# Kernel tuning notes

Hardware: AMD Instinct MI355X
Metric: run time of the kernel (lower is better)

## Reference

```python
import jax, jax.numpy as jnp
import numpy as np

N_DRUG = 50000
N_PROT = 50000
N_EDGE = 800000
D_IN = 256
D_HID = 256
D_OUT = 128


def setup_inputs() -> dict:
    key = jax.random.key(0)
    ks = jax.random.split(key, 20)
    s_in = 1.0 / np.sqrt(D_IN)
    inp = {
        'x_drug': jax.random.normal(ks[0], (N_DRUG, D_IN), jnp.float32),
        'x_protein': jax.random.normal(ks[1], (N_PROT, D_IN), jnp.float32),
        'edge_dp': jnp.stack([
            jax.random.randint(ks[2], (N_EDGE,), 0, N_DRUG, jnp.int32),
            jax.random.randint(ks[3], (N_EDGE,), 0, N_PROT, jnp.int32)]),
        'edge_pd': jnp.stack([
            jax.random.randint(ks[4], (N_EDGE,), 0, N_PROT, jnp.int32),
            jax.random.randint(ks[5], (N_EDGE,), 0, N_DRUG, jnp.int32)]),
        'W1l_dp': jax.random.normal(ks[6], (D_IN, D_HID), jnp.float32) * s_in,
        'W1r_dp': jax.random.normal(ks[7], (D_IN, D_HID), jnp.float32) * s_in,
        'b1_dp': jnp.zeros((D_HID,), jnp.float32),
        'W1l_pd': jax.random.normal(ks[8], (D_IN, D_HID), jnp.float32) * s_in,
        'W1r_pd': jax.random.normal(ks[9], (D_IN, D_HID), jnp.float32) * s_in,
        'b1_pd': jnp.zeros((D_HID,), jnp.float32),
        'W2l_dp': jax.random.normal(ks[10], (D_HID, D_OUT), jnp.float32) / np.sqrt(D_HID),
        'W2r_dp': jax.random.normal(ks[11], (D_HID, D_OUT), jnp.float32) / np.sqrt(D_HID),
        'b2_dp': jnp.zeros((D_OUT,), jnp.float32),
        'W2l_pd': jax.random.normal(ks[12], (D_HID, D_OUT), jnp.float32) / np.sqrt(D_HID),
        'W2r_pd': jax.random.normal(ks[13], (D_HID, D_OUT), jnp.float32) / np.sqrt(D_HID),
        'b2_pd': jnp.zeros((D_OUT,), jnp.float32),
    }
    return inp


def _sage(x_src, x_dst, edge, Wl, Wr, b):
    """PyG SAGEConv (mean aggr): lin_l(mean_neighbors) + lin_r(x_dst) + bias."""
    src, dst = edge[0], edge[1]
    n_dst = x_dst.shape[0]
    msg = x_src[src]                                        # [E, d] gather
    s = jax.ops.segment_sum(msg, dst, num_segments=n_dst)   # [n_dst, d]
    cnt = jax.ops.segment_sum(jnp.ones((edge.shape[1],), x_src.dtype), dst,
                              num_segments=n_dst)
    mean = s / jnp.maximum(cnt, 1.0)[:, None]
    return mean @ Wl + x_dst @ Wr + b


def _l2norm(x, eps=1e-12):
    n = jnp.sqrt(jnp.sum(x * x, axis=-1, keepdims=True))
    return x / jnp.maximum(n, eps)


def reference(x_drug, x_protein, edge_dp, edge_pd,
              W1l_dp, W1r_dp, b1_dp, W1l_pd, W1r_pd, b1_pd,
              W2l_dp, W2r_dp, b2_dp, W2l_pd, W2r_pd, b2_pd):
    # Layer 1 (HeteroConv, aggr='sum'; each node type has one incoming edge type)
    h_prot = _sage(x_drug, x_protein, edge_dp, W1l_dp, W1r_dp, b1_dp)
    h_drug = _sage(x_protein, x_drug, edge_pd, W1l_pd, W1r_pd, b1_pd)
    h_prot = jax.nn.relu(h_prot)  # dropout is identity in eval mode
    h_drug = jax.nn.relu(h_drug)
    # Layer 2 (output layer) + L2 normalize
    z_prot = _sage(h_drug, h_prot, edge_dp, W2l_dp, W2r_dp, b2_dp)
    z_drug = _sage(h_prot, h_drug, edge_pd, W2l_pd, W2r_pd, b2_pd)
    return _l2norm(z_drug), _l2norm(z_prot)
```

## Files before the change

kernel.cpp:

```cpp
#include <hip/hip_runtime.h>

typedef unsigned short u16;
typedef unsigned int u32;
typedef __attribute__((ext_vector_type(8))) short short8;
typedef __attribute__((ext_vector_type(4))) float f32x4;

#define NDIM 256
#define KCAT 512
#define EB 8192
#define NBK_MAX 256

__device__ __forceinline__ float bf2f(u16 u) {
  union { u32 i; float f; } v; v.i = ((u32)u) << 16; return v.f;
}
__device__ __forceinline__ u16 f2bf(float f) {
  union { float f; u32 i; } v; v.f = f;
  u32 u = v.i;
  u32 r = (u + 0x7fffu + ((u >> 16) & 1u)) >> 16;
  return (u16)r;
}

__global__ void cvt_f32_bf16_2(const float* __restrict__ a, int n4a,
                               const float* __restrict__ b, int n4b,
                               u16* __restrict__ oa, u16* __restrict__ ob) {
  int i = blockIdx.x * blockDim.x + threadIdx.x;
  const float* in; u16* out; int j;
  if (i < n4a) { in = a; out = oa; j = i; }
  else { j = i - n4a; if (j >= n4b) return; in = b; out = ob; }
  const float4 v = reinterpret_cast<const float4*>(in)[j];
  u32 lo = (u32)f2bf(v.x) | ((u32)f2bf(v.y) << 16);
  u32 hi = (u32)f2bf(v.z) | ((u32)f2bf(v.w) << 16);
  reinterpret_cast<uint2*>(out)[j] = make_uint2(lo, hi);
}

__global__ void prep_wcat(const float* __restrict__ Wl0, const float* __restrict__ Wr0,
                          u16* __restrict__ WT0,
                          const float* __restrict__ Wl1, const float* __restrict__ Wr1,
                          u16* __restrict__ WT1) {
  int idx = blockIdx.x * blockDim.x + threadIdx.x;
  if (idx >= 256 * KCAT) return;
  const float* Wl = blockIdx.y ? Wl1 : Wl0;
  const float* Wr = blockIdx.y ? Wr1 : Wr0;
  u16* WT = blockIdx.y ? WT1 : WT0;
  int n = idx >> 9, k = idx & 511;
  float v = (k < 256) ? Wl[k * 256 + n] : Wr[(k - 256) * 256 + n];
  WT[idx] = f2bf(v);
}

__global__ void prep_wcat2(const float* __restrict__ Wl0, const float* __restrict__ Wr0,
                           u16* __restrict__ WT0,
                           const float* __restrict__ Wl1, const float* __restrict__ Wr1,
                           u16* __restrict__ WT1) {
  int idx = blockIdx.x * blockDim.x + threadIdx.x;
  if (idx >= 256 * 256) return;
  const float* Wl = blockIdx.y ? Wl1 : Wl0;
  const float* Wr = blockIdx.y ? Wr1 : Wr0;
  u16* WT = blockIdx.y ? WT1 : WT0;
  int n = idx >> 8, k = idx & 255;
  float v = (n < 128) ? Wl[k * 128 + n] : Wr[k * 128 + (n - 128)];
  WT[idx] = f2bf(v);
}

__global__ void prep_fbias(const float* __restrict__ bd, const float* __restrict__ bp,
                           float* __restrict__ fd, float* __restrict__ fp) {
  int n = threadIdx.x;
  fd[n] = (n < 128) ? 0.f : bd[n - 128];
  fp[n] = (n < 128) ? 0.f : bp[n - 128];
}

#define SCAN_CHUNK 2048

__global__ void scan_p1(const int* __restrict__ c0, int n0,
                        const int* __restrict__ c1, int n1,
                        int* __restrict__ bsums) {
  const int sel = blockIdx.y;
  const int* c = sel ? c1 : c0;
  const int n = sel ? n1 : n0;
  const int base = blockIdx.x * SCAN_CHUNK;
  const int tid = threadIdx.x, lane = tid & 63, w = tid >> 6;
  int s = 0;
  const int i0 = base + tid * 8;
#pragma unroll
  for (int j = 0; j < 8; ++j) {
    int i = i0 + j;
    s += (i < n) ? c[i] : 0;
  }
#pragma unroll
  for (int d = 1; d < 64; d <<= 1) s += __shfl_xor(s, d, 64);
  __shared__ int wsum[4];
  if (lane == 0) wsum[w] = s;
  __syncthreads();
  if (tid == 0) bsums[sel * 64 + blockIdx.x] = wsum[0] + wsum[1] + wsum[2] + wsum[3];
}

__global__ void scan_p2(int* __restrict__ bsums, int nb) {
  const int sel = blockIdx.x;
  const int lane = threadIdx.x;
  int v = (lane < nb) ? bsums[sel * 64 + lane] : 0;
#pragma unroll
  for (int d = 1; d < 64; d <<= 1) {
    int t = __shfl_up(v, d, 64);
    if (lane >= d) v += t;
  }
  int ex = __shfl_up(v, 1, 64);
  if (lane == 0) ex = 0;
  if (lane < nb) bsums[sel * 64 + lane] = ex;
}

__global__ void scan_p3(const int* __restrict__ c0, int n0, int* __restrict__ off0,
                        const int* __restrict__ c1, int n1, int* __restrict__ off1,
                        const int* __restrict__ bsums) {
  const int sel = blockIdx.y;
  const int* c = sel ? c1 : c0;
  int* off = sel ? off1 : off0;
  const int n = sel ? n1 : n0;
  const int base = blockIdx.x * SCAN_CHUNK;
  const int tid = threadIdx.x, lane = tid & 63, w = tid >> 6;
  int v[8];
  int s = 0;
  const int i0 = base + tid * 8;
#pragma unroll
  for (int j = 0; j < 8; ++j) {
    int i = i0 + j;
    v[j] = (i < n) ? c[i] : 0;
    s += v[j];
  }
  int inc = s;
#pragma unroll
  for (int d = 1; d < 64; d <<= 1) {
    int t = __shfl_up(inc, d, 64);
    if (lane >= d) inc += t;
  }
  __shared__ int wsum[4];
  if (lane == 63) wsum[w] = inc;
  __syncthreads();
  int wbase = 0;
  for (int q = 0; q < w; ++q) wbase += wsum[q];
  int run = (inc - s) + wbase + bsums[sel * 64 + blockIdx.x];
#pragma unroll
  for (int j = 0; j < 8; ++j) {
    int i = i0 + j;
    run += v[j];
    if (i < n) off[i + 1] = run;
  }
  if (blockIdx.x == 0 && tid == 0) off[0] = 0;
}

__global__ void hist_pass(const int* __restrict__ d0, const int* __restrict__ d1, int E,
                          int nblk, int nbuckets, int* __restrict__ h0, int* __restrict__ h1) {
  const int sel = blockIdx.y;
  const int* dst = sel ? d1 : d0;
  int* hist = sel ? h1 : h0;
  const int blk = blockIdx.x;
  __shared__ int h[NBK_MAX];
  for (int b = threadIdx.x; b < nbuckets; b += 256) h[b] = 0;
  __syncthreads();
  const int e0 = blk * EB;
  const int e1 = (e0 + EB < E) ? (e0 + EB) : E;
  for (int i = e0 + threadIdx.x; i < e1; i += 256) atomicAdd(&h[dst[i] >> 8], 1);
  __syncthreads();
  for (int b = threadIdx.x; b < nbuckets; b += 256) hist[b * nblk + blk] = h[b];
}

__global__ void part_pass(const int* __restrict__ s0, const int* __restrict__ d0, u32* __restrict__ t0,
                          const int* __restrict__ s1, const int* __restrict__ d1, u32* __restrict__ t1,
                          const int* __restrict__ ho0, const int* __restrict__ ho1,
                          int E, int nblk, int nbuckets) {
  const int sel = blockIdx.y;
  const int* src = sel ? s1 : s0;
  const int* dst = sel ? d1 : d0;
  const int* hoff = sel ? ho1 : ho0;
  u32* tmp = sel ? t1 : t0;
  const int blk = blockIdx.x;
  __shared__ int cur[NBK_MAX];
  for (int b = threadIdx.x; b < nbuckets; b += 256) cur[b] = hoff[b * nblk + blk];
  __syncthreads();
  const int e0 = blk * EB;
  const int e1 = (e0 + EB < E) ? (e0 + EB) : E;
  for (int i = e0 + threadIdx.x; i < e1; i += 256) {
    const int d = dst[i];
    const int p = atomicAdd(&cur[d >> 8], 1);
    tmp[p] = ((u32)(d & 255) << 16) | (u32)src[i];
  }
}

__global__ void bucket_fill(const u32* __restrict__ t0, const int* __restrict__ ho0,
                            int n0, int* __restrict__ off0, int* __restrict__ l0,
                            const u32* __restrict__ t1, const int* __restrict__ ho1,
                            int n1, int* __restrict__ off1, int* __restrict__ l1,
                            int E, int nblk, int nbuckets) {
  const int sel = blockIdx.y;
  const u32* tmp = sel ? t1 : t0;
  const int* hoff = sel ? ho1 : ho0;
  const int n = sel ? n1 : n0;
  int* off = sel ? off1 : off0;
  int* lst = sel ? l1 : l0;
  const int b = blockIdx.x;
  const int node0 = b << 8;
  if (node0 >= n) return;
  const int nodes = (n - node0 < 256) ? (n - node0) : 256;
  const int base = hoff[b * nblk];
  const int bend = hoff[(b + 1) * nblk];
  const int t = threadIdx.x, lane = t & 63, w = t >> 6;
  __shared__ int cnt[256];
  __shared__ int wsum[4];
  cnt[t] = 0;
  __syncthreads();
  for (int i = base + t; i < bend; i += 256) atomicAdd(&cnt[tmp[i] >> 16], 1);
  __syncthreads();
  const int v = cnt[t];
  int inc = v;
#pragma unroll
  for (int d = 1; d < 64; d <<= 1) {
    int x = __shfl_up(inc, d, 64);
    if (lane >= d) inc += x;
  }
  if (lane == 63) wsum[w] = inc;
  __syncthreads();
  int wb = 0;
  for (int q = 0; q < w; ++q) wb += wsum[q];
  const int excl = base + (inc - v) + wb;
  __syncthreads();
  cnt[t] = excl;
  if (t < nodes) off[node0 + t] = excl;
  if (node0 + nodes == n && t == 0) off[n] = E;
  __syncthreads();
  for (int i = base + t; i < bend; i += 256) {
    const u32 pk = tmp[i];
    const int p = atomicAdd(&cnt[pk >> 16], 1);
    lst[p] = (int)(pk & 0xffffu);
  }
}

__global__ void seg_mean(const u16* __restrict__ f0, const int* __restrict__ o0,
                         const int* __restrict__ l0, u16* __restrict__ out0, int n0,
                         const u16* __restrict__ f1, const int* __restrict__ o1,
                         const int* __restrict__ l1, u16* __restrict__ out1, int n1) {
  const int sel = blockIdx.y;
  const u16* feat = sel ? f1 : f0;
  const int* off = sel ? o1 : o0;
  const int* lst = sel ? l1 : l0;
  u16* out = sel ? out1 : out0;
  const int ndst = sel ? n1 : n0;
  const int wid = threadIdx.x >> 6, lane = threadIdx.x & 63;
  const int node = blockIdx.x * 4 + wid;
  if (node >= ndst) return;
  const int s = off[node], e = off[node + 1];
  const int half = lane >> 5, hl = lane & 31;
  float a[8];
#pragma unroll
  for (int j = 0; j < 8; ++j) a[j] = 0.f;
  int i = s;
  for (; i + 16 <= e; i += 16) {
    int q[8];
#pragma unroll
    for (int j = 0; j < 8; ++j) q[j] = lst[i + 2 * j + half];
    uint4 v[8];
#pragma unroll
    for (int j = 0; j < 8; ++j)
      v[j] = *reinterpret_cast<const uint4*>(feat + (size_t)q[j] * NDIM + hl * 8);
#pragma unroll
    for (int j = 0; j < 8; ++j) {
      const u32 w[4] = {v[j].x, v[j].y, v[j].z, v[j].w};
#pragma unroll
      for (int c = 0; c < 4; ++c) {
        a[2 * c] += bf2f((u16)(w[c] & 0xffffu));
        a[2 * c + 1] += bf2f((u16)(w[c] >> 16));
      }
    }
  }
  for (; i + 8 <= e; i += 8) {
    int q[4];
#pragma unroll
    for (int j = 0; j < 4; ++j) q[j] = lst[i + 2 * j + half];
    uint4 v[4];
#pragma unroll
    for (int j = 0; j < 4; ++j)
      v[j] = *reinterpret_cast<const uint4*>(feat + (size_t)q[j] * NDIM + hl * 8);
#pragma unroll
    for (int j = 0; j < 4; ++j) {
      const u32 w[4] = {v[j].x, v[j].y, v[j].z, v[j].w};
#pragma unroll
      for (int c = 0; c < 4; ++c) {
        a[2 * c] += bf2f((u16)(w[c] & 0xffffu));
        a[2 * c + 1] += bf2f((u16)(w[c] >> 16));
      }
    }
  }
  for (; i < e; i += 2) {
    if (i + half < e) {
      const int q = lst[i + half];
      const uint4 v = *reinterpret_cast<const uint4*>(feat + (size_t)q * NDIM + hl * 8);
      const u32 w[4] = {v.x, v.y, v.z, v.w};
#pragma unroll
      for (int c = 0; c < 4; ++c) {
        a[2 * c] += bf2f((u16)(w[c] & 0xffffu));
        a[2 * c + 1] += bf2f((u16)(w[c] >> 16));
      }
    }
  }
#pragma unroll
  for (int j = 0; j < 8; ++j) a[j] += __shfl_xor(a[j], 32, 64);
  if (half == 0) {
    const float inv = (e > s) ? 1.f / (float)(e - s) : 0.f;
    uint4 o;
    o.x = (u32)f2bf(a[0] * inv) | ((u32)f2bf(a[1] * inv) << 16);
    o.y = (u32)f2bf(a[2] * inv) | ((u32)f2bf(a[3] * inv) << 16);
    o.z = (u32)f2bf(a[4] * inv) | ((u32)f2bf(a[5] * inv) << 16);
    o.w = (u32)f2bf(a[6] * inv) | ((u32)f2bf(a[7] * inv) << 16);
    *reinterpret_cast<uint4*>(out + (size_t)node * NDIM + hl * 8) = o;
  }
}

__global__ void seg_out(const u16* __restrict__ ym0, const u16* __restrict__ ys0,
                        const int* __restrict__ o0, const int* __restrict__ l0,
                        float* __restrict__ z0, int n0,
                        const u16* __restrict__ ym1, const u16* __restrict__ ys1,
                        const int* __restrict__ o1, const int* __restrict__ l1,
                        float* __restrict__ z1, int n1) {
  const int sel = blockIdx.y;
  const u16* ymsg = sel ? ym1 : ym0;
  const u16* yself = sel ? ys1 : ys0;
  const int* off = sel ? o1 : o0;
  const int* lst = sel ? l1 : l0;
  float* zout = sel ? z1 : z0;
  const int ndst = sel ? n1 : n0;
  const int wid = threadIdx.x >> 6, lane = threadIdx.x & 63;
  const int node = blockIdx.x * 4 + wid;
  if (node >= ndst) return;
  const int s = off[node], e = off[node + 1];
  const int q = lane >> 4, ql = lane & 15;
  float a[8];
#pragma unroll
  for (int j = 0; j < 8; ++j) a[j] = 0.f;
  int i = s;
  for (; i + 16 <= e; i += 16) {
    int r[4];
#pragma unroll
    for (int j = 0; j < 4; ++j) r[j] = lst[i + 4 * j + q];
    uint4 v[4];
#pragma unroll
    for (int j = 0; j < 4; ++j)
      v[j] = *reinterpret_cast<const uint4*>(ymsg + (size_t)r[j] * 256 + ql * 8);
#pragma unroll
    for (int j = 0; j < 4; ++j) {
      const u32 w[4] = {v[j].x, v[j].y, v[j].z, v[j].w};
#pragma unroll
      for (int c = 0; c < 4; ++c) {
        a[2 * c] += bf2f((u16)(w[c] & 0xffffu));
        a[2 * c + 1] += bf2f((u16)(w[c] >> 16));
      }
    }
  }
  for (; i + 4 <= e; i += 4) {
    const int r = lst[i + q];
    const uint4 v = *reinterpret_cast<const uint4*>(ymsg + (size_t)r * 256 + ql * 8);
    const u32 w[4] = {v.x, v.y, v.z, v.w};
#pragma unroll
    for (int c = 0; c < 4; ++c) {
      a[2 * c] += bf2f((u16)(w[c] & 0xffffu));
      a[2 * c + 1] += bf2f((u16)(w[c] >> 16));
    }
  }
  if (i + q < e) {
    const int r = lst[i + q];
    const uint4 v = *reinterpret_cast<const uint4*>(ymsg + (size_t)r * 256 + ql * 8);
    const u32 w[4] = {v.x, v.y, v.z, v.w};
#pragma unroll
    for (int c = 0; c < 4; ++c) {
      a[2 * c] += bf2f((u16)(w[c] & 0xffffu));
      a[2 * c + 1] += bf2f((u16)(w[c] >> 16));
    }
  }
#pragma unroll
  for (int j = 0; j < 8; ++j) {
    a[j] += __shfl_xor(a[j], 16, 64);
    a[j] += __shfl_xor(a[j], 32, 64);
  }
  const float inv = (e > s) ? 1.f / (float)(e - s) : 0.f;
  const uint4 r = *reinterpret_cast<const uint4*>(yself + (size_t)node * 256 + 128 + ql * 8);
  const u32 rw[4] = {r.x, r.y, r.z, r.w};
  float z[8];
  float ss = 0.f;
#pragma unroll
  for (int c = 0; c < 4; ++c) {
    z[2 * c] = a[2 * c] * inv + bf2f((u16)(rw[c] & 0xffffu));
    z[2 * c + 1] = a[2 * c + 1] * inv + bf2f((u16)(rw[c] >> 16));
    ss += z[2 * c] * z[2 * c] + z[2 * c + 1] * z[2 * c + 1];
  }
#pragma unroll
  for (int d = 1; d < 16; d <<= 1) ss += __shfl_xor(ss, d, 64);
  const float sc = 1.f / fmaxf(sqrtf(ss), 1e-12f);
  if (q == 0) {
    float4 o0v, o1v;
    o0v.x = z[0] * sc; o0v.y = z[1] * sc; o0v.z = z[2] * sc; o0v.w = z[3] * sc;
    o1v.x = z[4] * sc; o1v.y = z[5] * sc; o1v.z = z[6] * sc; o1v.w = z[7] * sc;
    float* zp = zout + (size_t)node * 128 + ql * 8;
    *reinterpret_cast<float4*>(zp) = o0v;
    *reinterpret_cast<float4*>(zp + 4) = o1v;
  }
}

template <bool RELU, bool CAT, int KT, typename OutT>
__global__ __launch_bounds__(256) void gemm_cat2(
    const u16* __restrict__ Am0, const u16* __restrict__ Ax0,
    const u16* __restrict__ WT0, const float* __restrict__ bias0,
    OutT* __restrict__ out0, int M0,
    const u16* __restrict__ Am1, const u16* __restrict__ Ax1,
    const u16* __restrict__ WT1, const float* __restrict__ bias1,
    OutT* __restrict__ out1, int M1,
    int ldb, int ldo) {
  const int sel = blockIdx.z;
  const u16* Am = sel ? Am1 : Am0;
  const u16* Ax = sel ? Ax1 : Ax0;
  const u16* WT = sel ? WT1 : WT0;
  const float* bias = sel ? bias1 : bias0;
  OutT* out = sel ? out1 : out0;
  const int M = sel ? M1 : M0;
  const int gm0 = blockIdx.x * 128;
  if (gm0 >= M) return;

  __shared__ u16 As[8 * 128 * 8];
  __shared__ u16 Bs[8 * 128 * 8];
  const int tid = threadIdx.x;
  const int wid = tid >> 6, lane = tid & 63;
  const int wr = wid >> 1, wc = wid & 1;
  const int n0 = blockIdx.y * 128;

  f32x4 acc[4][4];
  const f32x4 zz = {0.f, 0.f, 0.f, 0.f};
#pragma unroll
  for (int i = 0; i < 4; ++i)
#pragma unroll
    for (int j = 0; j < 4; ++j) acc[i][j] = zz;

  for (int kt = 0; kt < KT; ++kt) {
    const u16* Asrc = CAT ? ((kt < KT / 2) ? Am : Ax) : Am;
    const int koff = CAT ? ((kt & (KT / 2 - 1)) * 64) : kt * 64;
#pragma unroll
    for (int t = 0; t < 4; ++t) {
      int f = wid * 256 + t * 64 + lane;
      int c = f >> 7, r = f & 127;
      int grow = gm0 + r; grow = (grow < M) ? grow : (M - 1);
      const u16* g = Asrc + (size_t)grow * NDIM + koff + c * 8;
      u16* l = &As[(size_t)(wid * 256 + t * 64) * 8];
      __builtin_amdgcn_global_load_lds((const __attribute__((address_space(1))) void*)g,
                                       (__attribute__((address_space(3))) void*)l, 16, 0, 0);
    }
#pragma unroll
    for (int t = 0; t < 4; ++t) {
      int f = wid * 256 + t * 64 + lane;
      int c = f >> 7, n = f & 127;
      const u16* g = WT + (size_t)(n0 + n) * ldb + kt * 64 + c * 8;
      u16* l = &Bs[(size_t)(wid * 256 + t * 64) * 8];
      __builtin_amdgcn_global_load_lds((const __attribute__((address_space(1))) void*)g,
                                       (__attribute__((address_space(3))) void*)l, 16, 0, 0);
    }
    __syncthreads();
#pragma unroll
    for (int ks = 0; ks < 2; ++ks) {
      const int kc = ks * 4 + (lane >> 4);
      short8 a[4], b[4];
#pragma unroll
      for (int mt = 0; mt < 4; ++mt)
        a[mt] = *reinterpret_cast<const short8*>(
            &As[(size_t)(kc * 128 + wr * 64 + mt * 16 + (lane & 15)) * 8]);
#pragma unroll
      for (int nt = 0; nt < 4; ++nt)
        b[nt] = *reinterpret_cast<const short8*>(
            &Bs[(size_t)(kc * 128 + wc * 64 + nt * 16 + (lane & 15)) * 8]);
#pragma unroll
      for (int mt = 0; mt < 4; ++mt)
#pragma unroll
        for (int nt = 0; nt < 4; ++nt)
          acc[mt][nt] = __builtin_amdgcn_mfma_f32_16x16x32_bf16(a[mt], b[nt], acc[mt][nt], 0, 0, 0);
    }
    __syncthreads();
  }

  const int rw = gm0 + wr * 64;
#pragma unroll
  for (int mt = 0; mt < 4; ++mt) {
#pragma unroll
    for (int j = 0; j < 4; ++j) {
      int row = rw + mt * 16 + ((lane >> 4) << 2) + j;
      if (row >= M) continue;
#pragma unroll
      for (int nt = 0; nt < 4; ++nt) {
        int col = n0 + wc * 64 + nt * 16 + (lane & 15);
        float v = acc[mt][nt][j] + bias[col];
        if (RELU) v = fmaxf(v, 0.f);
        if constexpr (sizeof(OutT) == 2) out[(size_t)row * ldo + col] = f2bf(v);
        else out[(size_t)row * ldo + col] = v;
      }
    }
  }
}

extern "C" void kernel_launch(void* const* d_in, const int* in_sizes, int n_in,
                              void* d_out, int out_size, void* d_ws, size_t ws_size,
                              hipStream_t stream) {
  const float* x_drug = (const float*)d_in[0];
  const float* x_prot = (const float*)d_in[1];
  const int* e_dp = (const int*)d_in[2];
  const int* e_pd = (const int*)d_in[3];
  const float* W1l_dp = (const float*)d_in[4];
  const float* W1r_dp = (const float*)d_in[5];
  const float* b1_dp = (const float*)d_in[6];
  const float* W1l_pd = (const float*)d_in[7];
  const float* W1r_pd = (const float*)d_in[8];
  const float* b1_pd = (const float*)d_in[9];
  const float* W2l_dp = (const float*)d_in[10];
  const float* W2r_dp = (const float*)d_in[11];
  const float* b2_dp = (const float*)d_in[12];
  const float* W2l_pd = (const float*)d_in[13];
  const float* W2r_pd = (const float*)d_in[14];
  const float* b2_pd = (const float*)d_in[15];

  const int E = in_sizes[2] / 2;
  const int ND = in_sizes[0] / NDIM;
  const int NP = in_sizes[1] / NDIM;

  const int* dp_src = e_dp;
  const int* dp_dst = e_dp + E;
  const int* pd_src = e_pd;
  const int* pd_dst = e_pd + E;

  char* ws = (char*)d_ws;
  size_t o = 0;
  auto alloc = [&](size_t bytes) -> void* {
    void* p = ws + o;
    o = (o + bytes + 255) & ~(size_t)255;
    return p;
  };
  u16* xd16 = (u16*)alloc((size_t)ND * NDIM * 2);
  u16* xp16 = (u16*)alloc((size_t)NP * NDIM * 2);
  u16* mp16 = (u16*)alloc((size_t)NP * NDIM * 2);
  u16* md16 = (u16*)alloc((size_t)ND * NDIM * 2);
  u16* hp16 = (u16*)alloc((size_t)NP * NDIM * 2);
  u16* hd16 = (u16*)alloc((size_t)ND * NDIM * 2);
  u16* wt1dp = (u16*)alloc((size_t)256 * KCAT * 2);
  u16* wt1pd = (u16*)alloc((size_t)256 * KCAT * 2);
  u16* wt2d = (u16*)alloc((size_t)256 * 256 * 2);
  u16* wt2p = (u16*)alloc((size_t)256 * 256 * 2);
  float* fbias_d = (float*)alloc(256 * 4);
  float* fbias_p = (float*)alloc(256 * 4);
  int* off_dp = (int*)alloc((size_t)(NP + 1) * 4);
  int* off_pd = (int*)alloc((size_t)(ND + 1) * 4);
  int* bsums2 = (int*)alloc((size_t)2 * 64 * 4);
  int* lst_dp = (int*)alloc((size_t)E * 4);
  int* lst_pd = (int*)alloc((size_t)E * 4);
  u32* tmp_dp = (u32*)alloc((size_t)E * 4);
  u32* tmp_pd = (u32*)alloc((size_t)E * 4);

  const int nmax = (NP > ND) ? NP : ND;
  const int nbuckets = (nmax + 255) >> 8;
  const int nblk = (E + EB - 1) / EB;
  const int nh = nbuckets * nblk;
  int* hist0 = (int*)alloc((size_t)nh * 4);
  int* hist1 = (int*)alloc((size_t)nh * 4);
  int* hoff0 = (int*)alloc((size_t)(nh + 1) * 4);
  int* hoff1 = (int*)alloc((size_t)(nh + 1) * 4);

  dim3 blk(256);

  const int n4d = ND * NDIM / 4, n4p = NP * NDIM / 4;
  cvt_f32_bf16_2<<<(n4d + n4p + 255) / 256, blk, 0, stream>>>(x_drug, n4d, x_prot, n4p, xd16, xp16);

  prep_wcat<<<dim3((256 * KCAT + 255) / 256, 2), blk, 0, stream>>>(
      W1l_dp, W1r_dp, wt1dp, W1l_pd, W1r_pd, wt1pd);
  prep_wcat2<<<dim3((256 * 256 + 255) / 256, 2), blk, 0, stream>>>(
      W2l_dp, W2r_pd, wt2d, W2l_pd, W2r_dp, wt2p);
  prep_fbias<<<1, 256, 0, stream>>>(b2_pd, b2_dp, fbias_d, fbias_p);

  hist_pass<<<dim3(nblk, 2), blk, 0, stream>>>(dp_dst, pd_dst, E, nblk, nbuckets, hist0, hist1);
  const int nb2 = (nh + SCAN_CHUNK - 1) / SCAN_CHUNK;
  dim3 sg2(nb2, 2);
  scan_p1<<<sg2, blk, 0, stream>>>(hist0, nh, hist1, nh, bsums2);
  scan_p2<<<2, 64, 0, stream>>>(bsums2, nb2);
  scan_p3<<<sg2, blk, 0, stream>>>(hist0, nh, hoff0, hist1, nh, hoff1, bsums2);
  part_pass<<<dim3(nblk, 2), blk, 0, stream>>>(
      dp_src, dp_dst, tmp_dp, pd_src, pd_dst, tmp_pd, hoff0, hoff1, E, nblk, nbuckets);
  bucket_fill<<<dim3(nbuckets, 2), blk, 0, stream>>>(
      tmp_dp, hoff0, NP, off_dp, lst_dp, tmp_pd, hoff1, ND, off_pd, lst_pd, E, nblk, nbuckets);

  seg_mean<<<dim3((nmax + 3) / 4, 2), blk, 0, stream>>>(
      xd16, off_dp, lst_dp, mp16, NP, xp16, off_pd, lst_pd, md16, ND);

  const int gx = (nmax + 127) / 128;
  gemm_cat2<true, true, 8, u16><<<dim3(gx, 2, 2), blk, 0, stream>>>(
      mp16, xp16, wt1dp, b1_dp, hp16, NP,
      md16, xd16, wt1pd, b1_pd, hd16, ND, KCAT, 256);

  u16* yp16 = mp16;
  u16* yd16 = md16;
  gemm_cat2<false, false, 4, u16><<<dim3(gx, 2, 2), blk, 0, stream>>>(
      hd16, hd16, wt2d, fbias_d, yd16, ND,
      hp16, hp16, wt2p, fbias_p, yp16, NP, 256, 256);

  float* zd = (float*)d_out;
  float* zp = zd + (size_t)ND * 128;
  seg_out<<<dim3((nmax + 3) / 4, 2), blk, 0, stream>>>(
      yp16, yd16, off_pd, lst_pd, zd, ND, yd16, yp16, off_dp, lst_dp, zp, NP);
}
```

Before: 406.1 us.

## Split feature matrices into two 128-column halves for cache-friendly gathers

Input features and intermediate buffers are stored as separate low and high 128-column halves. The neighbor-mean gather now runs as two passes, each touching a half-size table, so each pass's working set fits the cache better. The layer-2 GEMM writes its message and self outputs into separate compact buffers, and seg_out reads 128-wide rows. The cost is an extra kernel launch, an index-list reread in the second gather pass, and more pointer plumbing in the GEMM.

New measurement: 421.6 us. +3.8%, slower.

```diff
diff --git a/kernel.cpp b/kernel.cpp
--- a/kernel.cpp
+++ b/kernel.cpp
@@ -20,17 +20,20 @@
   return (u16)r;
 }
 
-__global__ void cvt_f32_bf16_2(const float* __restrict__ a, int n4a,
-                               const float* __restrict__ b, int n4b,
-                               u16* __restrict__ oa, u16* __restrict__ ob) {
+__global__ void cvt_split_2(const float* __restrict__ a, int n4a,
+                            const float* __restrict__ b, int n4b,
+                            u16* __restrict__ alo, u16* __restrict__ ahi,
+                            u16* __restrict__ blo, u16* __restrict__ bhi) {
   int i = blockIdx.x * blockDim.x + threadIdx.x;
-  const float* in; u16* out; int j;
-  if (i < n4a) { in = a; out = oa; j = i; }
-  else { j = i - n4a; if (j >= n4b) return; in = b; out = ob; }
+  const float* in; u16* lo; u16* hi; int j;
+  if (i < n4a) { in = a; lo = alo; hi = ahi; j = i; }
+  else { j = i - n4a; if (j >= n4b) return; in = b; lo = blo; hi = bhi; }
   const float4 v = reinterpret_cast<const float4*>(in)[j];
-  u32 lo = (u32)f2bf(v.x) | ((u32)f2bf(v.y) << 16);
-  u32 hi = (u32)f2bf(v.z) | ((u32)f2bf(v.w) << 16);
-  reinterpret_cast<uint2*>(out)[j] = make_uint2(lo, hi);
+  u32 w0 = (u32)f2bf(v.x) | ((u32)f2bf(v.y) << 16);
+  u32 w1 = (u32)f2bf(v.z) | ((u32)f2bf(v.w) << 16);
+  const int node = j >> 6, c4 = (j & 63) * 4;
+  u16* out = (c4 < 128) ? (lo + (size_t)node * 128 + c4) : (hi + (size_t)node * 128 + c4 - 128);
+  *reinterpret_cast<uint2*>(out) = make_uint2(w0, w1);
 }
 
 __global__ void prep_wcat(const float* __restrict__ Wl0, const float* __restrict__ Wr0,
@@ -232,10 +235,10 @@
   }
 }
 
-__global__ void seg_mean(const u16* __restrict__ f0, const int* __restrict__ o0,
-                         const int* __restrict__ l0, u16* __restrict__ out0, int n0,
-                         const u16* __restrict__ f1, const int* __restrict__ o1,
-                         const int* __restrict__ l1, u16* __restrict__ out1, int n1) {
+__global__ void seg_mean_h(const u16* __restrict__ f0, const int* __restrict__ o0,
+                           const int* __restrict__ l0, u16* __restrict__ out0, int n0,
+                           const u16* __restrict__ f1, const int* __restrict__ o1,
+                           const int* __restrict__ l1, u16* __restrict__ out1, int n1) {
   const int sel = blockIdx.y;
   const u16* feat = sel ? f1 : f0;
   const int* off = sel ? o1 : o0;
@@ -246,69 +249,56 @@
   const int node = blockIdx.x * 4 + wid;
   if (node >= ndst) return;
   const int s = off[node], e = off[node + 1];
-  const int half = lane >> 5, hl = lane & 31;
+  const int q = lane >> 4, ql = lane & 15;
   float a[8];
 #pragma unroll
   for (int j = 0; j < 8; ++j) a[j] = 0.f;
   int i = s;
-  for (; i + 16 <= e; i += 16) {
-    int q[8];
-#pragma unroll
-    for (int j = 0; j < 8; ++j) q[j] = lst[i + 2 * j + half];
-    uint4 v[8];
-#pragma unroll
-    for (int j = 0; j < 8; ++j)
-      v[j] = *reinterpret_cast<const uint4*>(feat + (size_t)q[j] * NDIM + hl * 8);
-#pragma unroll
-    for (int j = 0; j < 8; ++j) {
-      const u32 w[4] = {v[j].x, v[j].y, v[j].z, v[j].w};
-#pragma unroll
-      for (int c = 0; c < 4; ++c) {
-        a[2 * c] += bf2f((u16)(w[c] & 0xffffu));
-        a[2 * c + 1] += bf2f((u16)(w[c] >> 16));
-      }
-    }
-  }
   for (; i + 8 <= e; i += 8) {
-    int q[4];
-#pragma unroll
-    for (int j = 0; j < 4; ++j) q[j] = lst[i + 2 * j + half];
-    uint4 v[4];
-#pragma unroll
-    for (int j = 0; j < 4; ++j)
-      v[j] = *reinterpret_cast<const uint4*>(feat + (size_t)q[j] * NDIM + hl * 8);
-#pragma unroll
-    for (int j = 0; j < 4; ++j) {
-      const u32 w[4] = {v[j].x, v[j].y, v[j].z, v[j].w};
-#pragma unroll
-      for (int c = 0; c < 4; ++c) {
-        a[2 * c] += bf2f((u16)(w[c] & 0xffffu));
-        a[2 * c + 1] += bf2f((u16)(w[c] >> 16));
-      }
-    }
-  }
-  for (; i < e; i += 2) {
-    if (i + half < e) {
-      const int q = lst[i + half];
-      const uint4 v = *reinterpret_cast<const uint4*>(feat + (size_t)q * NDIM + hl * 8);
-      const u32 w[4] = {v.x, v.y, v.z, v.w};
-#pragma unroll
-      for (int c = 0; c < 4; ++c) {
-        a[2 * c] += bf2f((u16)(w[c] & 0xffffu));
-        a[2 * c + 1] += bf2f((u16)(w[c] >> 16));
-      }
-    }
-  }
-#pragma unroll
-  for (int j = 0; j < 8; ++j) a[j] += __shfl_xor(a[j], 32, 64);
-  if (half == 0) {
+    const int r0 = lst[i + q], r1 = lst[i + 4 + q];
+    const uint4 v0 = *reinterpret_cast<const uint4*>(feat + (size_t)r0 * 128 + ql * 8);
+    const uint4 v1 = *reinterpret_cast<const uint4*>(feat + (size_t)r1 * 128 + ql * 8);
+    const u32 w0[4] = {v0.x, v0.y, v0.z, v0.w};
+    const u32 w1[4] = {v1.x, v1.y, v1.z, v1.w};
+#pragma unroll
+    for (int c = 0; c < 4; ++c) {
+      a[2 * c] += bf2f((u16)(w0[c] & 0xffffu)) + bf2f((u16)(w1[c] & 0xffffu));
+      a[2 * c + 1] += bf2f((u16)(w0[c] >> 16)) + bf2f((u16)(w1[c] >> 16));
+    }
+  }
+  for (; i + 4 <= e; i += 4) {
+    const int r = lst[i + q];
+    const uint4 v = *reinterpret_cast<const uint4*>(feat + (size_t)r * 128 + ql * 8);
+    const u32 w[4] = {v.x, v.y, v.z, v.w};
+#pragma unroll
+    for (int c = 0; c < 4; ++c) {
+      a[2 * c] += bf2f((u16)(w[c] & 0xffffu));
+      a[2 * c + 1] += bf2f((u16)(w[c] >> 16));
+    }
+  }
+  if (i + q < e) {
+    const int r = lst[i + q];
+    const uint4 v = *reinterpret_cast<const uint4*>(feat + (size_t)r * 128 + ql * 8);
+    const u32 w[4] = {v.x, v.y, v.z, v.w};
+#pragma unroll
+    for (int c = 0; c < 4; ++c) {
+      a[2 * c] += bf2f((u16)(w[c] & 0xffffu));
+      a[2 * c + 1] += bf2f((u16)(w[c] >> 16));
+    }
+  }
+#pragma unroll
+  for (int j = 0; j < 8; ++j) {
+    a[j] += __shfl_xor(a[j], 16, 64);
+    a[j] += __shfl_xor(a[j], 32, 64);
+  }
+  if (q == 0) {
     const float inv = (e > s) ? 1.f / (float)(e - s) : 0.f;
     uint4 o;
     o.x = (u32)f2bf(a[0] * inv) | ((u32)f2bf(a[1] * inv) << 16);
     o.y = (u32)f2bf(a[2] * inv) | ((u32)f2bf(a[3] * inv) << 16);
     o.z = (u32)f2bf(a[4] * inv) | ((u32)f2bf(a[5] * inv) << 16);
     o.w = (u32)f2bf(a[6] * inv) | ((u32)f2bf(a[7] * inv) << 16);
-    *reinterpret_cast<uint4*>(out + (size_t)node * NDIM + hl * 8) = o;
+    *reinterpret_cast<uint4*>(out + (size_t)node * 128 + ql * 8) = o;
   }
 }
 
@@ -334,27 +324,21 @@
 #pragma unroll
   for (int j = 0; j < 8; ++j) a[j] = 0.f;
   int i = s;
-  for (; i + 16 <= e; i += 16) {
-    int r[4];
-#pragma unroll
-    for (int j = 0; j < 4; ++j) r[j] = lst[i + 4 * j + q];
-    uint4 v[4];
-#pragma unroll
-    for (int j = 0; j < 4; ++j)
-      v[j] = *reinterpret_cast<const uint4*>(ymsg + (size_t)r[j] * 256 + ql * 8);
-#pragma unroll
-    for (int j = 0; j < 4; ++j) {
-      const u32 w[4] = {v[j].x, v[j].y, v[j].z, v[j].w};
-#pragma unroll
-      for (int c = 0; c < 4; ++c) {
-        a[2 * c] += bf2f((u16)(w[c] & 0xffffu));
-        a[2 * c + 1] += bf2f((u16)(w[c] >> 16));
-      }
+  for (; i + 8 <= e; i += 8) {
+    const int r0 = lst[i + q], r1 = lst[i + 4 + q];
+    const uint4 v0 = *reinterpret_cast<const uint4*>(ymsg + (size_t)r0 * 128 + ql * 8);
+    const uint4 v1 = *reinterpret_cast<const uint4*>(ymsg + (size_t)r1 * 128 + ql * 8);
+    const u32 w0[4] = {v0.x, v0.y, v0.z, v0.w};
+    const u32 w1[4] = {v1.x, v1.y, v1.z, v1.w};
+#pragma unroll
+    for (int c = 0; c < 4; ++c) {
+      a[2 * c] += bf2f((u16)(w0[c] & 0xffffu)) + bf2f((u16)(w1[c] & 0xffffu));
+      a[2 * c + 1] += bf2f((u16)(w0[c] >> 16)) + bf2f((u16)(w1[c] >> 16));
     }
   }
   for (; i + 4 <= e; i += 4) {
     const int r = lst[i + q];
-    const uint4 v = *reinterpret_cast<const uint4*>(ymsg + (size_t)r * 256 + ql * 8);
+    const uint4 v = *reinterpret_cast<const uint4*>(ymsg + (size_t)r * 128 + ql * 8);
     const u32 w[4] = {v.x, v.y, v.z, v.w};
 #pragma unroll
     for (int c = 0; c < 4; ++c) {
@@ -364,7 +348,7 @@
   }
   if (i + q < e) {
     const int r = lst[i + q];
-    const uint4 v = *reinterpret_cast<const uint4*>(ymsg + (size_t)r * 256 + ql * 8);
+    const uint4 v = *reinterpret_cast<const uint4*>(ymsg + (size_t)r * 128 + ql * 8);
     const u32 w[4] = {v.x, v.y, v.z, v.w};
 #pragma unroll
     for (int c = 0; c < 4; ++c) {
@@ -378,7 +362,7 @@
     a[j] += __shfl_xor(a[j], 32, 64);
   }
   const float inv = (e > s) ? 1.f / (float)(e - s) : 0.f;
-  const uint4 r = *reinterpret_cast<const uint4*>(yself + (size_t)node * 256 + 128 + ql * 8);
+  const uint4 r = *reinterpret_cast<const uint4*>(yself + (size_t)node * 128 + ql * 8);
   const u32 rw[4] = {r.x, r.y, r.z, r.w};
   float z[8];
   float ss = 0.f;
@@ -401,26 +385,28 @@
   }
 }
 
-template <bool RELU, bool CAT, int KT, typename OutT>
+template <bool RELU, bool CAT, int KT, bool SPLIT, typename OutT>
 __global__ __launch_bounds__(256) void gemm_cat2(
-    const u16* __restrict__ Am0, const u16* __restrict__ Ax0,
+    const u16* __restrict__ A00, const u16* __restrict__ A01,
+    const u16* __restrict__ A02, const u16* __restrict__ A03,
     const u16* __restrict__ WT0, const float* __restrict__ bias0,
-    OutT* __restrict__ out0, int M0,
-    const u16* __restrict__ Am1, const u16* __restrict__ Ax1,
+    OutT* __restrict__ out0, OutT* __restrict__ outs0, int M0,
+    const u16* __restrict__ A10, const u16* __restrict__ A11,
+    const u16* __restrict__ A12, const u16* __restrict__ A13,
     const u16* __restrict__ WT1, const float* __restrict__ bias1,
-    OutT* __restrict__ out1, int M1,
+    OutT* __restrict__ out1, OutT* __restrict__ outs1, int M1,
     int ldb, int ldo) {
   const int sel = blockIdx.z;
-  const u16* Am = sel ? Am1 : Am0;
-  const u16* Ax = sel ? Ax1 : Ax0;
+  const u16* As4[4] = {sel ? A10 : A00, sel ? A11 : A01, sel ? A12 : A02, sel ? A13 : A03};
   const u16* WT = sel ? WT1 : WT0;
   const float* bias = sel ? bias1 : bias0;
   OutT* out = sel ? out1 : out0;
+  OutT* outs = sel ? outs1 : outs0;
   const int M = sel ? M1 : M0;
   const int gm0 = blockIdx.x * 128;
   if (gm0 >= M) return;
 
-  __shared__ u16 As[8 * 128 * 8];
+  __shared__ u16 Asm[8 * 128 * 8];
   __shared__ u16 Bs[8 * 128 * 8];
   const int tid = threadIdx.x;
   const int wid = tid >> 6, lane = tid & 63;
@@ -435,15 +421,16 @@
     for (int j = 0; j < 4; ++j) acc[i][j] = zz;
 
   for (int kt = 0; kt < KT; ++kt) {
-    const u16* Asrc = CAT ? ((kt < KT / 2) ? Am : Ax) : Am;
-    const int koff = CAT ? ((kt & (KT / 2 - 1)) * 64) : kt * 64;
+    const u16* Asrc = CAT ? As4[kt >> 1] : As4[0];
+    const int koff = CAT ? ((kt & 1) * 64) : kt * 64;
+    const int lda = CAT ? 128 : NDIM;
 #pragma unroll
     for (int t = 0; t < 4; ++t) {
       int f = wid * 256 + t * 64 + lane;
       int c = f >> 7, r = f & 127;
       int grow = gm0 + r; grow = (grow < M) ? grow : (M - 1);
-      const u16* g = Asrc + (size_t)grow * NDIM + koff + c * 8;
-      u16* l = &As[(size_t)(wid * 256 + t * 64) * 8];
+      const u16* g = Asrc + (size_t)grow * lda + koff + c * 8;
+      u16* l = &Asm[(size_t)(wid * 256 + t * 64) * 8];
       __builtin_amdgcn_global_load_lds((const __attribute__((address_space(1))) void*)g,
                                        (__attribute__((address_space(3))) void*)l, 16, 0, 0);
     }
@@ -464,7 +451,7 @@
 #pragma unroll
       for (int mt = 0; mt < 4; ++mt)
         a[mt] = *reinterpret_cast<const short8*>(
-            &As[(size_t)(kc * 128 + wr * 64 + mt * 16 + (lane & 15)) * 8]);
+            &Asm[(size_t)(kc * 128 + wr * 64 + mt * 16 + (lane & 15)) * 8]);
 #pragma unroll
       for (int nt = 0; nt < 4; ++nt)
         b[nt] = *reinterpret_cast<const short8*>(
@@ -490,8 +477,14 @@
         int col = n0 + wc * 64 + nt * 16 + (lane & 15);
         float v = acc[mt][nt][j] + bias[col];
         if (RELU) v = fmaxf(v, 0.f);
-        if constexpr (sizeof(OutT) == 2) out[(size_t)row * ldo + col] = f2bf(v);
-        else out[(size_t)row * ldo + col] = v;
+        if constexpr (SPLIT) {
+          if (col < 128) out[(size_t)row * 128 + col] = f2bf(v);
+          else outs[(size_t)row * 128 + col - 128] = f2bf(v);
+        } else if constexpr (sizeof(OutT) == 2) {
+          out[(size_t)row * ldo + col] = f2bf(v);
+        } else {
+          out[(size_t)row * ldo + col] = v;
+        }
       }
     }
   }
@@ -533,10 +526,14 @@
     o = (o + bytes + 255) & ~(size_t)255;
     return p;
   };
-  u16* xd16 = (u16*)alloc((size_t)ND * NDIM * 2);
-  u16* xp16 = (u16*)alloc((size_t)NP * NDIM * 2);
-  u16* mp16 = (u16*)alloc((size_t)NP * NDIM * 2);
-  u16* md16 = (u16*)alloc((size_t)ND * NDIM * 2);
+  u16* xdlo = (u16*)alloc((size_t)ND * 128 * 2);
+  u16* xdhi = (u16*)alloc((size_t)ND * 128 * 2);
+  u16* xplo = (u16*)alloc((size_t)NP * 128 * 2);
+  u16* xphi = (u16*)alloc((size_t)NP * 128 * 2);
+  u16* mplo = (u16*)alloc((size_t)NP * 128 * 2);
+  u16* mphi = (u16*)alloc((size_t)NP * 128 * 2);
+  u16* mdlo = (u16*)alloc((size_t)ND * 128 * 2);
+  u16* mdhi = (u16*)alloc((size_t)ND * 128 * 2);
   u16* hp16 = (u16*)alloc((size_t)NP * NDIM * 2);
   u16* hd16 = (u16*)alloc((size_t)ND * NDIM * 2);
   u16* wt1dp = (u16*)alloc((size_t)256 * KCAT * 2);
@@ -565,7 +562,8 @@
   dim3 blk(256);
 
   const int n4d = ND * NDIM / 4, n4p = NP * NDIM / 4;
-  cvt_f32_bf16_2<<<(n4d + n4p + 255) / 256, blk, 0, stream>>>(x_drug, n4d, x_prot, n4p, xd16, xp16);
+  cvt_split_2<<<(n4d + n4p + 255) / 256, blk, 0, stream>>>(
+      x_drug, n4d, x_prot, n4p, xdlo, xdhi, xplo, xphi);
 
   prep_wcat<<<dim3((256 * KCAT + 255) / 256, 2), blk, 0, stream>>>(
       W1l_dp, W1r_dp, wt1dp, W1l_pd, W1r_pd, wt1pd);
@@ -584,22 +582,27 @@
   bucket_fill<<<dim3(nbuckets, 2), blk, 0, stream>>>(
       tmp_dp, hoff0, NP, off_dp, lst_dp, tmp_pd, hoff1, ND, off_pd, lst_pd, E, nblk, nbuckets);
 
-  seg_mean<<<dim3((nmax + 3) / 4, 2), blk, 0, stream>>>(
-      xd16, off_dp, lst_dp, mp16, NP, xp16, off_pd, lst_pd, md16, ND);
+  dim3 sgm((nmax + 3) / 4, 2);
+  seg_mean_h<<<sgm, blk, 0, stream>>>(
+      xdlo, off_dp, lst_dp, mplo, NP, xplo, off_pd, lst_pd, mdlo, ND);
+  seg_mean_h<<<sgm, blk, 0, stream>>>(
+      xdhi, off_dp, lst_dp, mphi, NP, xphi, off_pd, lst_pd, mdhi, ND);
 
   const int gx = (nmax + 127) / 128;
-  gemm_cat2<true, true, 8, u16><<<dim3(gx, 2, 2), blk, 0, stream>>>(
-      mp16, xp16, wt1dp, b1_dp, hp16, NP,
-      md16, xd16, wt1pd, b1_pd, hd16, ND, KCAT, 256);
-
-  u16* yp16 = mp16;
-  u16* yd16 = md16;
-  gemm_cat2<false, false, 4, u16><<<dim3(gx, 2, 2), blk, 0, stream>>>(
-      hd16, hd16, wt2d, fbias_d, yd16, ND,
-      hp16, hp16, wt2p, fbias_p, yp16, NP, 256, 256);
+  gemm_cat2<true, true, 8, false, u16><<<dim3(gx, 2, 2), blk, 0, stream>>>(
+      mplo, mphi, xplo, xphi, wt1dp, b1_dp, hp16, (u16*)nullptr, NP,
+      mdlo, mdhi, xdlo, xdhi, wt1pd, b1_pd, hd16, (u16*)nullptr, ND, KCAT, 256);
+
+  u16* ymsg_d = mdlo;
+  u16* yself_d = mdhi;
+  u16* ymsg_p = mplo;
+  u16* yself_p = mphi;
+  gemm_cat2<false, false, 4, true, u16><<<dim3(gx, 2, 2), blk, 0, stream>>>(
+      hd16, hd16, hd16, hd16, wt2d, fbias_d, ymsg_d, yself_d, ND,
+      hp16, hp16, hp16, hp16, wt2p, fbias_p, ymsg_p, yself_p, NP, 256, 256);
 
   float* zd = (float*)d_out;
   float* zp = zd + (size_t)ND * 128;
   seg_out<<<dim3((nmax + 3) / 4, 2), blk, 0, stream>>>(
-      yp16, yd16, off_pd, lst_pd, zd, ND, yd16, yp16, off_dp, lst_dp, zp, NP);
-}
+      ymsg_p, yself_d, off_pd, lst_pd, zd, ND, ymsg_d, yself_p, off_dp, lst_dp, zp, NP);
+}
```

## Double-buffer GEMM LDS tiles, remap blocks across XCDs, split layer-2 outputs compactly

Applied to the files above, without the earlier changes.

The GEMM now stages the next K tile into a second LDS buffer while computing the current one, which removes one barrier stall per iteration. Blocks are remapped so that consecutive M tiles land on different XCDs, and the two N halves of one tile share an XCD so the A rows get reused in its L2. Layer-2 output is written as two compact 128-wide arrays (message part and self part), so seg_out gathers rows of half the stride. The gather loops are also reshaped with shallower unrolls and tree-style adds. Doubling the LDS use may lower occupancy, and the smaller unroll exposes less memory-level parallelism in the gathers.

Result: slower. 430.1 us (+5.9%).

```diff
diff --git a/kernel.cpp b/kernel.cpp
--- a/kernel.cpp
+++ b/kernel.cpp
@@ -251,40 +251,23 @@
 #pragma unroll
   for (int j = 0; j < 8; ++j) a[j] = 0.f;
   int i = s;
-  for (; i + 16 <= e; i += 16) {
-    int q[8];
-#pragma unroll
-    for (int j = 0; j < 8; ++j) q[j] = lst[i + 2 * j + half];
-    uint4 v[8];
-#pragma unroll
-    for (int j = 0; j < 8; ++j)
-      v[j] = *reinterpret_cast<const uint4*>(feat + (size_t)q[j] * NDIM + hl * 8);
-#pragma unroll
-    for (int j = 0; j < 8; ++j) {
-      const u32 w[4] = {v[j].x, v[j].y, v[j].z, v[j].w};
-#pragma unroll
-      for (int c = 0; c < 4; ++c) {
-        a[2 * c] += bf2f((u16)(w[c] & 0xffffu));
-        a[2 * c + 1] += bf2f((u16)(w[c] >> 16));
-      }
-    }
-  }
   for (; i + 8 <= e; i += 8) {
-    int q[4];
-#pragma unroll
-    for (int j = 0; j < 4; ++j) q[j] = lst[i + 2 * j + half];
-    uint4 v[4];
-#pragma unroll
-    for (int j = 0; j < 4; ++j)
-      v[j] = *reinterpret_cast<const uint4*>(feat + (size_t)q[j] * NDIM + hl * 8);
-#pragma unroll
-    for (int j = 0; j < 4; ++j) {
-      const u32 w[4] = {v[j].x, v[j].y, v[j].z, v[j].w};
-#pragma unroll
-      for (int c = 0; c < 4; ++c) {
-        a[2 * c] += bf2f((u16)(w[c] & 0xffffu));
-        a[2 * c + 1] += bf2f((u16)(w[c] >> 16));
-      }
+    const int q0 = lst[i + half], q1 = lst[i + 2 + half];
+    const int q2 = lst[i + 4 + half], q3 = lst[i + 6 + half];
+    const uint4 v0 = *reinterpret_cast<const uint4*>(feat + (size_t)q0 * NDIM + hl * 8);
+    const uint4 v1 = *reinterpret_cast<const uint4*>(feat + (size_t)q1 * NDIM + hl * 8);
+    const uint4 v2 = *reinterpret_cast<const uint4*>(feat + (size_t)q2 * NDIM + hl * 8);
+    const uint4 v3 = *reinterpret_cast<const uint4*>(feat + (size_t)q3 * NDIM + hl * 8);
+    const u32 w0[4] = {v0.x, v0.y, v0.z, v0.w};
+    const u32 w1[4] = {v1.x, v1.y, v1.z, v1.w};
+    const u32 w2[4] = {v2.x, v2.y, v2.z, v2.w};
+    const u32 w3[4] = {v3.x, v3.y, v3.z, v3.w};
+#pragma unroll
+    for (int q = 0; q < 4; ++q) {
+      a[2 * q] += bf2f((u16)(w0[q] & 0xffffu)) + bf2f((u16)(w1[q] & 0xffffu)) +
+                  bf2f((u16)(w2[q] & 0xffffu)) + bf2f((u16)(w3[q] & 0xffffu));
+      a[2 * q + 1] += bf2f((u16)(w0[q] >> 16)) + bf2f((u16)(w1[q] >> 16)) +
+                      bf2f((u16)(w2[q] >> 16)) + bf2f((u16)(w3[q] >> 16));
     }
   }
   for (; i < e; i += 2) {
@@ -293,9 +276,9 @@
       const uint4 v = *reinterpret_cast<const uint4*>(feat + (size_t)q * NDIM + hl * 8);
       const u32 w[4] = {v.x, v.y, v.z, v.w};
 #pragma unroll
-      for (int c = 0; c < 4; ++c) {
-        a[2 * c] += bf2f((u16)(w[c] & 0xffffu));
-        a[2 * c + 1] += bf2f((u16)(w[c] >> 16));
+      for (int t = 0; t < 4; ++t) {
+        a[2 * t] += bf2f((u16)(w[t] & 0xffffu));
+        a[2 * t + 1] += bf2f((u16)(w[t] >> 16));
       }
     }
   }
@@ -334,27 +317,21 @@
 #pragma unroll
   for (int j = 0; j < 8; ++j) a[j] = 0.f;
   int i = s;
-  for (; i + 16 <= e; i += 16) {
-    int r[4];
-#pragma unroll
-    for (int j = 0; j < 4; ++j) r[j] = lst[i + 4 * j + q];
-    uint4 v[4];
-#pragma unroll
-    for (int j = 0; j < 4; ++j)
-      v[j] = *reinterpret_cast<const uint4*>(ymsg + (size_t)r[j] * 256 + ql * 8);
-#pragma unroll
-    for (int j = 0; j < 4; ++j) {
-      const u32 w[4] = {v[j].x, v[j].y, v[j].z, v[j].w};
-#pragma unroll
-      for (int c = 0; c < 4; ++c) {
-        a[2 * c] += bf2f((u16)(w[c] & 0xffffu));
-        a[2 * c + 1] += bf2f((u16)(w[c] >> 16));
-      }
+  for (; i + 8 <= e; i += 8) {
+    const int r0 = lst[i + q], r1 = lst[i + 4 + q];
+    const uint4 v0 = *reinterpret_cast<const uint4*>(ymsg + (size_t)r0 * 128 + ql * 8);
+    const uint4 v1 = *reinterpret_cast<const uint4*>(ymsg + (size_t)r1 * 128 + ql * 8);
+    const u32 w0[4] = {v0.x, v0.y, v0.z, v0.w};
+    const u32 w1[4] = {v1.x, v1.y, v1.z, v1.w};
+#pragma unroll
+    for (int c = 0; c < 4; ++c) {
+      a[2 * c] += bf2f((u16)(w0[c] & 0xffffu)) + bf2f((u16)(w1[c] & 0xffffu));
+      a[2 * c + 1] += bf2f((u16)(w0[c] >> 16)) + bf2f((u16)(w1[c] >> 16));
     }
   }
   for (; i + 4 <= e; i += 4) {
     const int r = lst[i + q];
-    const uint4 v = *reinterpret_cast<const uint4*>(ymsg + (size_t)r * 256 + ql * 8);
+    const uint4 v = *reinterpret_cast<const uint4*>(ymsg + (size_t)r * 128 + ql * 8);
     const u32 w[4] = {v.x, v.y, v.z, v.w};
 #pragma unroll
     for (int c = 0; c < 4; ++c) {
@@ -364,7 +341,7 @@
   }
   if (i + q < e) {
     const int r = lst[i + q];
-    const uint4 v = *reinterpret_cast<const uint4*>(ymsg + (size_t)r * 256 + ql * 8);
+    const uint4 v = *reinterpret_cast<const uint4*>(ymsg + (size_t)r * 128 + ql * 8);
     const u32 w[4] = {v.x, v.y, v.z, v.w};
 #pragma unroll
     for (int c = 0; c < 4; ++c) {
@@ -378,7 +355,7 @@
     a[j] += __shfl_xor(a[j], 32, 64);
   }
   const float inv = (e > s) ? 1.f / (float)(e - s) : 0.f;
-  const uint4 r = *reinterpret_cast<const uint4*>(yself + (size_t)node * 256 + 128 + ql * 8);
+  const uint4 r = *reinterpret_cast<const uint4*>(yself + (size_t)node * 128 + ql * 8);
   const u32 rw[4] = {r.x, r.y, r.z, r.w};
   float z[8];
   float ss = 0.f;
@@ -401,31 +378,37 @@
   }
 }
 
-template <bool RELU, bool CAT, int KT, typename OutT>
-__global__ __launch_bounds__(256) void gemm_cat2(
+template <bool RELU, bool CAT, int KT, bool SPLIT>
+__global__ __launch_bounds__(256) void gemm2(
     const u16* __restrict__ Am0, const u16* __restrict__ Ax0,
     const u16* __restrict__ WT0, const float* __restrict__ bias0,
-    OutT* __restrict__ out0, int M0,
+    u16* __restrict__ out0, u16* __restrict__ outs0, int M0,
     const u16* __restrict__ Am1, const u16* __restrict__ Ax1,
     const u16* __restrict__ WT1, const float* __restrict__ bias1,
-    OutT* __restrict__ out1, int M1,
-    int ldb, int ldo) {
+    u16* __restrict__ out1, u16* __restrict__ outs1, int M1,
+    int gx, int ldb, int ldo) {
+  const int raw = blockIdx.x;
+  const int xcd = raw & 7, seq = raw >> 3;
+  const int ny = seq & 1;
+  const int mt = (seq >> 1) * 8 + xcd;
+  if (mt >= gx) return;
   const int sel = blockIdx.z;
   const u16* Am = sel ? Am1 : Am0;
   const u16* Ax = sel ? Ax1 : Ax0;
   const u16* WT = sel ? WT1 : WT0;
   const float* bias = sel ? bias1 : bias0;
-  OutT* out = sel ? out1 : out0;
+  u16* out = sel ? out1 : out0;
+  u16* outs = sel ? outs1 : outs0;
   const int M = sel ? M1 : M0;
-  const int gm0 = blockIdx.x * 128;
+  const int gm0 = mt * 128;
   if (gm0 >= M) return;
-
-  __shared__ u16 As[8 * 128 * 8];
-  __shared__ u16 Bs[8 * 128 * 8];
+  const int n0 = ny * 128;
+
+  __shared__ u16 As[2][8192];
+  __shared__ u16 Bs[2][8192];
   const int tid = threadIdx.x;
   const int wid = tid >> 6, lane = tid & 63;
   const int wr = wid >> 1, wc = wid & 1;
-  const int n0 = blockIdx.y * 128;
 
   f32x4 acc[4][4];
   const f32x4 zz = {0.f, 0.f, 0.f, 0.f};
@@ -434,7 +417,7 @@
 #pragma unroll
     for (int j = 0; j < 4; ++j) acc[i][j] = zz;
 
-  for (int kt = 0; kt < KT; ++kt) {
+  auto stage = [&](int kt, int buf) {
     const u16* Asrc = CAT ? ((kt < KT / 2) ? Am : Ax) : Am;
     const int koff = CAT ? ((kt & (KT / 2 - 1)) * 64) : kt * 64;
 #pragma unroll
@@ -443,7 +426,7 @@
       int c = f >> 7, r = f & 127;
       int grow = gm0 + r; grow = (grow < M) ? grow : (M - 1);
       const u16* g = Asrc + (size_t)grow * NDIM + koff + c * 8;
-      u16* l = &As[(size_t)(wid * 256 + t * 64) * 8];
+      u16* l = &As[buf][(size_t)(wid * 256 + t * 64) * 8];
       __builtin_amdgcn_global_load_lds((const __attribute__((address_space(1))) void*)g,
                                        (__attribute__((address_space(3))) void*)l, 16, 0, 0);
     }
@@ -452,46 +435,57 @@
       int f = wid * 256 + t * 64 + lane;
       int c = f >> 7, n = f & 127;
       const u16* g = WT + (size_t)(n0 + n) * ldb + kt * 64 + c * 8;
-      u16* l = &Bs[(size_t)(wid * 256 + t * 64) * 8];
+      u16* l = &Bs[buf][(size_t)(wid * 256 + t * 64) * 8];
       __builtin_amdgcn_global_load_lds((const __attribute__((address_space(1))) void*)g,
                                        (__attribute__((address_space(3))) void*)l, 16, 0, 0);
     }
-    __syncthreads();
+  };
+
+  stage(0, 0);
+  __syncthreads();
+
+  for (int kt = 0; kt < KT; ++kt) {
+    const int cur = kt & 1;
+    if (kt + 1 < KT) stage(kt + 1, cur ^ 1);
 #pragma unroll
     for (int ks = 0; ks < 2; ++ks) {
       const int kc = ks * 4 + (lane >> 4);
       short8 a[4], b[4];
 #pragma unroll
-      for (int mt = 0; mt < 4; ++mt)
-        a[mt] = *reinterpret_cast<const short8*>(
-            &As[(size_t)(kc * 128 + wr * 64 + mt * 16 + (lane & 15)) * 8]);
+      for (int mtt = 0; mtt < 4; ++mtt)
+        a[mtt] = *reinterpret_cast<const short8*>(
+            &As[cur][(size_t)(kc * 128 + wr * 64 + mtt * 16 + (lane & 15)) * 8]);
 #pragma unroll
       for (int nt = 0; nt < 4; ++nt)
         b[nt] = *reinterpret_cast<const short8*>(
-            &Bs[(size_t)(kc * 128 + wc * 64 + nt * 16 + (lane & 15)) * 8]);
-#pragma unroll
-      for (int mt = 0; mt < 4; ++mt)
+            &Bs[cur][(size_t)(kc * 128 + wc * 64 + nt * 16 + (lane & 15)) * 8]);
+#pragma unroll
+      for (int mtt = 0; mtt < 4; ++mtt)
 #pragma unroll
         for (int nt = 0; nt < 4; ++nt)
-          acc[mt][nt] = __builtin_amdgcn_mfma_f32_16x16x32_bf16(a[mt], b[nt], acc[mt][nt], 0, 0, 0);
+          acc[mtt][nt] = __builtin_amdgcn_mfma_f32_16x16x32_bf16(a[mtt], b[nt], acc[mtt][nt], 0, 0, 0);
     }
     __syncthreads();
   }
 
   const int rw = gm0 + wr * 64;
 #pragma unroll
-  for (int mt = 0; mt < 4; ++mt) {
+  for (int mtt = 0; mtt < 4; ++mtt) {
 #pragma unroll
     for (int j = 0; j < 4; ++j) {
-      int row = rw + mt * 16 + ((lane >> 4) << 2) + j;
+      int row = rw + mtt * 16 + ((lane >> 4) << 2) + j;
       if (row >= M) continue;
 #pragma unroll
       for (int nt = 0; nt < 4; ++nt) {
         int col = n0 + wc * 64 + nt * 16 + (lane & 15);
-        float v = acc[mt][nt][j] + bias[col];
+        float v = acc[mtt][nt][j] + bias[col];
         if (RELU) v = fmaxf(v, 0.f);
-        if constexpr (sizeof(OutT) == 2) out[(size_t)row * ldo + col] = f2bf(v);
-        else out[(size_t)row * ldo + col] = v;
+        if constexpr (SPLIT) {
+          if (col < 128) out[(size_t)row * 128 + col] = f2bf(v);
+          else outs[(size_t)row * 128 + col - 128] = f2bf(v);
+        } else {
+          out[(size_t)row * ldo + col] = f2bf(v);
+        }
       }
     }
   }
@@ -588,18 +582,22 @@
       xd16, off_dp, lst_dp, mp16, NP, xp16, off_pd, lst_pd, md16, ND);
 
   const int gx = (nmax + 127) / 128;
-  gemm_cat2<true, true, 8, u16><<<dim3(gx, 2, 2), blk, 0, stream>>>(
-      mp16, xp16, wt1dp, b1_dp, hp16, NP,
-      md16, xd16, wt1pd, b1_pd, hd16, ND, KCAT, 256);
-
-  u16* yp16 = mp16;
-  u16* yd16 = md16;
-  gemm_cat2<false, false, 4, u16><<<dim3(gx, 2, 2), blk, 0, stream>>>(
-      hd16, hd16, wt2d, fbias_d, yd16, ND,
-      hp16, hp16, wt2p, fbias_p, yp16, NP, 256, 256);
+  const int gridx = ((gx + 7) / 8) * 16;
+
+  gemm2<true, true, 8, false><<<dim3(gridx, 1, 2), blk, 0, stream>>>(
+      mp16, xp16, wt1dp, b1_dp, hp16, (u16*)nullptr, NP,
+      md16, xd16, wt1pd, b1_pd, hd16, (u16*)nullptr, ND, gx, KCAT, 256);
+
+  u16* ymsg_d = md16;
+  u16* yself_d = md16 + (size_t)ND * 128;
+  u16* ymsg_p = mp16;
+  u16* yself_p = mp16 + (size_t)NP * 128;
+  gemm2<false, false, 4, true><<<dim3(gridx, 1, 2), blk, 0, stream>>>(
+      hd16, hd16, wt2d, fbias_d, ymsg_d, yself_d, ND,
+      hp16, hp16, wt2p, fbias_p, ymsg_p, yself_p, NP, gx, 256, 256);
 
   float* zd = (float*)d_out;
   float* zp = zd + (size_t)ND * 128;
   seg_out<<<dim3((nmax + 3) / 4, 2), blk, 0, stream>>>(
-      yp16, yd16, off_pd, lst_pd, zd, ND, yd16, yp16, off_dp, lst_dp, zp, NP);
-}
+      ymsg_p, yself_d, off_pd, lst_pd, zd, ND, ymsg_d, yself_p, off_dp, lst_dp, zp, NP);
+}
```
